# Optimization experiments

Hardware: AMD Instinct MI355X
Metric: run time of the kernel (lower is better)

The kernel has to match this reference:

```python
import jax, jax.numpy as jnp
import numpy as np

D = 64       # embedding_dim
N = 10000    # nodes
E = 160000   # edges (avg degree 16)
R = 16       # removals
C = 512      # connected edges scored per removal


def setup_inputs() -> dict:
    key = jax.random.key(0)
    ks = jax.random.split(key, 18)
    coords = jax.random.normal(ks[0], (N, 2), jnp.float32)
    edge_src = jax.random.randint(ks[1], (E,), 0, N, jnp.int32)
    edge_dst = jax.random.randint(ks[2], (E,), 0, N, jnp.int32)
    removal_idx = jax.random.randint(ks[3], (R,), 0, N, jnp.int32)
    conn_eidx = jax.random.randint(ks[4], (R, C), 0, E, jnp.int32)
    s2 = 1.0 / np.sqrt(2.0)
    sD = 1.0 / np.sqrt(D)
    s2D = 1.0 / np.sqrt(2 * D)
    return {
        "coords": coords,
        "W_emb": jax.random.normal(ks[5], (2, D), jnp.float32) * s2,
        "b_emb": jnp.zeros((D,), jnp.float32),
        "W_self0": jax.random.normal(ks[6], (D, D), jnp.float32) * sD,
        "W_neigh0": jax.random.normal(ks[7], (D, D), jnp.float32) * sD,
        "b_gnn0": jnp.zeros((D,), jnp.float32),
        "W_self1": jax.random.normal(ks[8], (D, D), jnp.float32) * sD,
        "W_neigh1": jax.random.normal(ks[9], (D, D), jnp.float32) * sD,
        "b_gnn1": jnp.zeros((D,), jnp.float32),
        "W_edge": jax.random.normal(ks[10], (2 * D, D), jnp.float32) * s2D,
        "b_edge": jnp.zeros((D,), jnp.float32),
        "W_score": jax.random.normal(ks[11], (2 * D, 1), jnp.float32) * s2D,
        "b_score": jnp.zeros((1,), jnp.float32),
        "edge_src": edge_src,
        "edge_dst": edge_dst,
        "removal_idx": removal_idx,
        "conn_eidx": conn_eidx,
    }


def reference(coords, W_emb, b_emb, W_self0, W_neigh0, b_gnn0,
              W_self1, W_neigh1, b_gnn1, W_edge, b_edge, W_score, b_score,
              edge_src, edge_dst, removal_idx, conn_eidx):
    Nn = coords.shape[0]
    h0 = coords @ W_emb + b_emb  # [N, D] init node embedding

    def gnn_layer(h, emask, Ws, Wn, b):
        # masked mean aggregation of neighbor messages, then linear + relu
        msg = h[edge_src] * emask[:, None]                       # [E, D]
        agg = jax.ops.segment_sum(msg, edge_dst, num_segments=Nn)
        deg = jax.ops.segment_sum(emask, edge_dst, num_segments=Nn)
        agg = agg / jnp.maximum(deg, 1.0)[:, None]
        return jax.nn.relu(h @ Ws + agg @ Wn + b)

    def per_removal(r, conn):
        # tempDestroy: mask out removed node's participation in message passing
        nmask = jnp.ones((Nn,), coords.dtype).at[r].set(0.0)
        emask = nmask[edge_src] * nmask[edge_dst]                # [E]
        h = h0
        h = gnn_layer(h, emask, W_self0, W_neigh0, b_gnn0) + h   # residual
        h = gnn_layer(h, emask, W_self1, W_neigh1, b_gnn1) + h
        s, d = edge_src[conn], edge_dst[conn]                    # connected edges
        ef = jax.nn.relu(jnp.concatenate([h[s], h[d]], -1) @ W_edge + b_edge)  # [C, D]
        r_embed = coords[r] @ W_emb + b_emb                      # [D]
        score_in = jnp.concatenate(
            [jnp.broadcast_to(r_embed, (conn.shape[0], r_embed.shape[0])), ef], -1)
        score = score_in @ W_score + b_score                     # [C, 1]
        return jax.nn.softmax(score, axis=0)[:, 0]               # softmax over edges

    return jax.vmap(per_removal)(removal_idx, conn_eidx)         # [R, C]
```

## Files before the change

### kernel.cpp

```cpp
#include <hip/hip_runtime.h>

#define Df 64
#define NN 10000
#define EE 160000
#define RR 16
#define CC 512
#define CAP1 128
#define CAP2 2048
#define NGEMM 157
#define NAGG 2500
#define NEDG 625
#define NSLF 40
#define ND1B 512
#define ND2B 8192

__device__ float g_h0[NN * Df];
__device__ float g_h1b[NN * Df];
__device__ float g_h2b[NN * Df];
__device__ float g_agg[NN * Df];
__device__ float g_zrow[Df];
__device__ __align__(16) float g_W20[128 * Df];
__device__ __align__(16) float g_W21[128 * Df];
__device__ int g_cntI[NN], g_rowI[NN + 1], g_posI[NN], g_csrI[EE];
__device__ int g_m1mask[NN], g_m2mask[NN];
__device__ int g_mark1[RR][NN], g_mark2[RR][NN];
__device__ int g_n1[RR], g_n2[RR];
__device__ int g_list1[RR][CAP1], g_list2[RR][CAP2];
__device__ float g_d1[RR][CAP1][Df];
__device__ float g_d2[RR][CAP2][Df];
__device__ float g_score[RR * CC];

__global__ void k_init(const float* __restrict__ coords, const float* __restrict__ We,
                       const float* __restrict__ be, const float* __restrict__ Ws0,
                       const float* __restrict__ Wn0, const float* __restrict__ Ws1,
                       const float* __restrict__ Wn1) {
    int i = blockIdx.x * 256 + threadIdx.x;
    if (i < NN * Df) {
        int n = i >> 6, d = i & 63;
        g_h0[i] = coords[2 * n] * We[d] + coords[2 * n + 1] * We[Df + d] + be[d];
    }
    if (i < NN) { g_cntI[i] = 0; g_m1mask[i] = 0; g_m2mask[i] = 0; }
    if (i < Df) g_zrow[i] = 0.f;
    if (i < 8192) {
        int k = i >> 6, d = i & 63;
        g_W20[i] = (k < 64) ? Ws0[k * 64 + d] : Wn0[(k - 64) * 64 + d];
    } else if (i < 16384) {
        int i2 = i - 8192;
        int k = i2 >> 6, d = i2 & 63;
        g_W21[i2] = (k < 64) ? Ws1[k * 64 + d] : Wn1[(k - 64) * 64 + d];
    }
}

__global__ void k_hist(const int* __restrict__ dst) {
    int e = blockIdx.x * 256 + threadIdx.x;
    if (e < EE) atomicAdd(&g_cntI[dst[e]], 1);
}

__global__ __launch_bounds__(1024) void k_scan() {
    int t = threadIdx.x;
    int lane = t & 63, wv = t >> 6;
    const int PER = 10;
    int base = t * PER;
    int vals[PER]; int loc = 0;
#pragma unroll
    for (int k = 0; k < PER; k++) { int v = base + k; vals[k] = (v < NN) ? g_cntI[v] : 0; loc += vals[k]; }
    int sc = loc;
#pragma unroll
    for (int off = 1; off < 64; off <<= 1) { int x = __shfl_up(sc, off, 64); if (lane >= off) sc += x; }
    __shared__ int wsum[16];
    if (lane == 63) wsum[wv] = sc;
    __syncthreads();
    if (t < 16) {
        int x = wsum[t]; int s2 = x;
#pragma unroll
        for (int off = 1; off < 16; off <<= 1) { int y = __shfl_up(s2, off, 16); if (t >= off) s2 += y; }
        wsum[t] = s2 - x;
    }
    __syncthreads();
    int run = wsum[wv] + (sc - loc);
#pragma unroll
    for (int k = 0; k < PER; k++) {
        int v = base + k;
        if (v < NN) { g_rowI[v] = run; g_posI[v] = run; run += vals[k]; }
    }
    if (t == 1023) g_rowI[NN] = run;
}

__global__ void k_fill(const int* __restrict__ src, const int* __restrict__ dst) {
    int e = blockIdx.x * 256 + threadIdx.x;
    if (e < EE) {
        int p = atomicAdd(&g_posI[dst[e]], 1);
        g_csrI[p] = src[e];
    }
}

__device__ __forceinline__ void compact256(const int* __restrict__ maskArr, int bit,
                                           int* mark, int* list, int* nout, int cap) {
    int t = threadIdx.x;
    int lane = t & 63, wv = t >> 6;
    const int PER = 40;
    int base = t * PER;
    int loc = 0;
    for (int k = 0; k < PER; k++) { int v = base + k; if (v < NN) loc += (maskArr[v] >> bit) & 1; }
    int sc = loc;
#pragma unroll
    for (int off = 1; off < 64; off <<= 1) { int x = __shfl_up(sc, off, 64); if (lane >= off) sc += x; }
    __shared__ int wsum[4];
    if (lane == 63) wsum[wv] = sc;
    __syncthreads();
    if (t == 0) { int a = 0; for (int w2 = 0; w2 < 4; w2++) { int x = wsum[w2]; wsum[w2] = a; a += x; } }
    __syncthreads();
    int run = wsum[wv] + (sc - loc);
    for (int k = 0; k < PER; k++) {
        int v = base + k;
        if (v < NN) {
            int f = (maskArr[v] >> bit) & 1;
            if (f && run < cap) { list[run] = v; mark[v] = run + 1; }
            else mark[v] = 0;
            run += f;
        }
    }
    if (t == 255) *nout = (run < cap) ? run : cap;
}

__device__ __forceinline__ void agg_quad(const float* __restrict__ hin, int b, int tid) {
    int lane = tid & 63, w = tid >> 6;
    int n = b * 4 + w;
    int a0 = g_rowI[n], a1 = g_rowI[n + 1];
    float s0 = 0.f, s1 = 0.f, s2 = 0.f, s3 = 0.f;
    int i = a0;
    for (; i + 4 <= a1; i += 4) {
        int c0 = g_csrI[i], c1 = g_csrI[i + 1], c2 = g_csrI[i + 2], c3 = g_csrI[i + 3];
        s0 += hin[c0 * Df + lane];
        s1 += hin[c1 * Df + lane];
        s2 += hin[c2 * Df + lane];
        s3 += hin[c3 * Df + lane];
    }
    for (; i < a1; i++) s0 += hin[g_csrI[i] * Df + lane];
    float s = (s0 + s1) + (s2 + s3);
    g_agg[n * Df + lane] = s / fmaxf((float)(a1 - a0), 1.f);
}

__device__ __forceinline__ void gemm_tile(const float* __restrict__ hin,
                                          float* __restrict__ hout,
                                          const float* __restrict__ W2,
                                          const float* __restrict__ bias, int m0,
                                          int tid) {
    __shared__ float Xs[32][68];
    __shared__ float Wl[32][64];
    int tx = tid & 15, ty = tid >> 4;
    float acc[4][4];
#pragma unroll
    for (int i = 0; i < 4; i++)
#pragma unroll
        for (int j = 0; j < 4; j++) acc[i][j] = 0.f;

    for (int c = 0; c < 4; c++) {
        const float* src = (c < 2) ? hin : g_agg;
        int kb = (c & 1) * 32;
        int kbase = c * 32;
#pragma unroll
        for (int rep = 0; rep < 2; rep++) {
            int slot = tid + rep * 256;
            int m = slot >> 3, q = slot & 7;
            int n = m0 + m;
            float4 v = make_float4(0.f, 0.f, 0.f, 0.f);
            if (n < NN) v = *(const float4*)&src[n * Df + kb + q * 4];
            Xs[q * 4 + 0][m] = v.x; Xs[q * 4 + 1][m] = v.y;
            Xs[q * 4 + 2][m] = v.z; Xs[q * 4 + 3][m] = v.w;
            int k = slot >> 4, dq = slot & 15;
            *(float4*)&Wl[k][dq * 4] = *(const float4*)&W2[(kbase + k) * Df + dq * 4];
        }
        __syncthreads();
#pragma unroll
        for (int k = 0; k < 32; k++) {
            float4 x4 = *(const float4*)&Xs[k][ty * 4];
            float4 w4 = *(const float4*)&Wl[k][tx * 4];
            float xs[4] = {x4.x, x4.y, x4.z, x4.w};
            float ws[4] = {w4.x, w4.y, w4.z, w4.w};
#pragma unroll
            for (int i = 0; i < 4; i++)
#pragma unroll
                for (int j = 0; j < 4; j++) acc[i][j] += xs[i] * ws[j];
        }
        __syncthreads();
    }
    float4 b4 = *(const float4*)&bias[tx * 4];
    float bb[4] = {b4.x, b4.y, b4.z, b4.w};
#pragma unroll
    for (int i = 0; i < 4; i++) {
        int n = m0 + ty * 4 + i;
        if (n < NN) {
            float4 hv = *(const float4*)&hin[n * Df + tx * 4];
            float4 o;
            o.x = fmaxf(acc[i][0] + bb[0], 0.f) + hv.x;
            o.y = fmaxf(acc[i][1] + bb[1], 0.f) + hv.y;
            o.z = fmaxf(acc[i][2] + bb[2], 0.f) + hv.z;
            o.w = fmaxf(acc[i][3] + bb[3], 0.f) + hv.w;
            *(float4*)&hout[n * Df + tx * 4] = o;
        }
    }
}

__global__ __launch_bounds__(256) void k_s1(const int* __restrict__ removal,
                                            const int* __restrict__ esrc,
                                            const int* __restrict__ edst) {
    int b = blockIdx.x, tid = threadIdx.x;
    if (b < NAGG) { agg_quad(g_h0, b, tid); return; }
    if (b < NAGG + NEDG) {
        int e = (b - NAGG) * 256 + tid;
        if (e < EE) {
            int s = esrc[e], d = edst[e];
            int m = 0;
#pragma unroll
            for (int ri = 0; ri < RR; ri++)
                if (s == removal[ri]) m |= (1 << ri);
            if (m) atomicOr(&g_m1mask[d], m);
        }
        return;
    }
    if (tid < RR) atomicOr(&g_m1mask[removal[tid]], 1 << tid);
}

__global__ __launch_bounds__(256) void k_s2(const float* __restrict__ b0,
                                            const int* __restrict__ esrc,
                                            const int* __restrict__ edst) {
    int b = blockIdx.x, tid = threadIdx.x;
    if (b < NGEMM) { gemm_tile(g_h0, g_h1b, g_W20, b0, b * 64, tid); return; }
    if (b < NGEMM + RR) {
        int ri = b - NGEMM;
        compact256(g_m1mask, ri, g_mark1[ri], g_list1[ri], &g_n1[ri], CAP1);
        return;
    }
    if (b < NGEMM + RR + NEDG) {
        int e = (b - NGEMM - RR) * 256 + tid;
        if (e < EE) {
            int m = g_m1mask[esrc[e]];
            if (m) atomicOr(&g_m2mask[edst[e]], m);
        }
        return;
    }
    int v = (b - NGEMM - RR - NEDG) * 256 + tid;
    if (v < NN) {
        int m = g_m1mask[v];
        if (m) atomicOr(&g_m2mask[v], m);
    }
}

__global__ __launch_bounds__(256) void k_s3(const int* __restrict__ removal,
        const float* __restrict__ Ws0, const float* __restrict__ Wn0,
        const float* __restrict__ b0) {
    int b = blockIdx.x, tid = threadIdx.x;
    if (b < NAGG) { agg_quad(g_h1b, b, tid); return; }
    if (b < NAGG + ND1B) {
        __shared__ float s_h[4][Df], s_a[4][Df];
        int rel = b - NAGG;
        int ri = rel >> 5, y = rel & 31;
        int lane = tid & 63, w = tid >> 6;
        int j = y * 4 + w;
        if (j >= g_n1[ri]) return;
        int v = g_list1[ri][j];
        int r = removal[ri];
        float p0s = 0.f, p1s = 0.f, p2s = 0.f, p3s = 0.f; int cnt = 0;
        if (v != r) {
            int e0 = g_rowI[v], e1 = g_rowI[v + 1];
            int i = e0;
            for (; i + 4 <= e1; i += 4) {
                int c0 = g_csrI[i], c1 = g_csrI[i + 1], c2 = g_csrI[i + 2], c3 = g_csrI[i + 3];
                const float* p0 = (c0 == r) ? g_zrow : &g_h0[c0 * Df];
                const float* p1 = (c1 == r) ? g_zrow : &g_h0[c1 * Df];
                const float* p2 = (c2 == r) ? g_zrow : &g_h0[c2 * Df];
                const float* p3 = (c3 == r) ? g_zrow : &g_h0[c3 * Df];
                p0s += p0[lane]; p1s += p1[lane]; p2s += p2[lane]; p3s += p3[lane];
                cnt += (c0 != r) + (c1 != r) + (c2 != r) + (c3 != r);
            }
            for (; i < e1; i++) {
                int c = g_csrI[i];
                const float* p = (c == r) ? g_zrow : &g_h0[c * Df];
                p0s += p[lane]; cnt += (c != r);
            }
        }
        float aggd = (p0s + p1s) + (p2s + p3s);
        float hv = g_h0[v * Df + lane];
        s_h[w][lane] = hv;
        s_a[w][lane] = aggd / fmaxf((float)cnt, 1.f);
        float acc = b0[lane];
#pragma unroll 16
        for (int k = 0; k < Df; k++)
            acc += s_h[w][k] * Ws0[k * Df + lane] + s_a[w][k] * Wn0[k * Df + lane];
        g_d1[ri][j][lane] = fmaxf(acc, 0.f) + hv;
        return;
    }
    int ri = b - NAGG - ND1B;
    compact256(g_m2mask, ri, g_mark2[ri], g_list2[ri], &g_n2[ri], CAP2);
}

__global__ __launch_bounds__(256) void k_s4(const int* __restrict__ removal,
        const float* __restrict__ Ws1, const float* __restrict__ Wn1,
        const float* __restrict__ b1) {
    int b = blockIdx.x, tid = threadIdx.x;
    if (b < NGEMM) { gemm_tile(g_h1b, g_h2b, g_W21, b1, b * 64, tid); return; }
    __shared__ float s_h[4][Df], s_a[4][Df];
    int rel = b - NGEMM;
    int ri = rel >> 9, y = rel & 511;
    int lane = tid & 63, w = tid >> 6;
    int j = y * 4 + w;
    if (j >= g_n2[ri]) return;
    int v = g_list2[ri][j];
    int r = removal[ri];
    const int* mk1 = g_mark1[ri];
    float p0s = 0.f, p1s = 0.f, p2s = 0.f, p3s = 0.f; int cnt = 0;
    if (v != r) {
        int e0 = g_rowI[v], e1 = g_rowI[v + 1];
        int i = e0;
        for (; i + 4 <= e1; i += 4) {
            int c0 = g_csrI[i], c1 = g_csrI[i + 1], c2 = g_csrI[i + 2], c3 = g_csrI[i + 3];
            int m0 = mk1[c0], m1 = mk1[c1], m2 = mk1[c2], m3 = mk1[c3];
            const float* p0 = (c0 == r) ? g_zrow : (m0 > 0 ? &g_d1[ri][m0 - 1][0] : &g_h1b[c0 * Df]);
            const float* p1 = (c1 == r) ? g_zrow : (m1 > 0 ? &g_d1[ri][m1 - 1][0] : &g_h1b[c1 * Df]);
            const float* p2 = (c2 == r) ? g_zrow : (m2 > 0 ? &g_d1[ri][m2 - 1][0] : &g_h1b[c2 * Df]);
            const float* p3 = (c3 == r) ? g_zrow : (m3 > 0 ? &g_d1[ri][m3 - 1][0] : &g_h1b[c3 * Df]);
            p0s += p0[lane]; p1s += p1[lane]; p2s += p2[lane]; p3s += p3[lane];
            cnt += (c0 != r) + (c1 != r) + (c2 != r) + (c3 != r);
        }
        for (; i < e1; i++) {
            int c = g_csrI[i];
            int m = mk1[c];
            const float* p = (c == r) ? g_zrow : (m > 0 ? &g_d1[ri][m - 1][0] : &g_h1b[c * Df]);
            p0s += p[lane]; cnt += (c != r);
        }
    }
    float aggd = (p0s + p1s) + (p2s + p3s);
    int mv = mk1[v];
    float hv = (mv > 0) ? g_d1[ri][mv - 1][lane] : g_h1b[v * Df + lane];
    s_h[w][lane] = hv;
    s_a[w][lane] = aggd / fmaxf((float)cnt, 1.f);
    float acc = b1[lane];
#pragma unroll 16
    for (int k = 0; k < Df; k++)
        acc += s_h[w][k] * Ws1[k * Df + lane] + s_a[w][k] * Wn1[k * Df + lane];
    g_d2[ri][j][lane] = fmaxf(acc, 0.f) + hv;
}

__global__ __launch_bounds__(256) void k_score(const int* __restrict__ conn,
        const int* __restrict__ removal, const int* __restrict__ esrc,
        const int* __restrict__ edst, const float* __restrict__ We,
        const float* __restrict__ be, const float* __restrict__ Wsc,
        const float* __restrict__ bsc) {
    __shared__ const float* ptrs[128];
    __shared__ float Xs[32][68];
    __shared__ float Wl[32][64];
    __shared__ float su;
    int tid = threadIdx.x;
    int e0 = blockIdx.x * 64;
    int ri = e0 >> 9;

    if (tid < 64) {
        int e = conn[e0 + tid];
        int s = esrc[e], d = edst[e];
        int ms = g_mark2[ri][s], md = g_mark2[ri][d];
        ptrs[tid]      = (ms > 0) ? &g_d2[ri][ms - 1][0] : &g_h2b[s * Df];
        ptrs[64 + tid] = (md > 0) ? &g_d2[ri][md - 1][0] : &g_h2b[d * Df];
    } else if (tid < 128) {
        int lane = tid & 63;
        float up = g_h0[removal[ri] * Df + lane] * Wsc[lane];
#pragma unroll
        for (int off = 32; off > 0; off >>= 1) up += __shfl_xor(up, off, 64);
        if (lane == 0) su = up;
    }
    __syncthreads();

    int tx = tid & 15, ty = tid >> 4;
    float acc[4][4];
#pragma unroll
    for (int i = 0; i < 4; i++)
#pragma unroll
        for (int j = 0; j < 4; j++) acc[i][j] = 0.f;

    for (int c = 0; c < 4; c++) {
        int kb = (c & 1) * 32;
#pragma unroll
        for (int rep = 0; rep < 2; rep++) {
            int slot = tid + rep * 256;
            int m = slot >> 3, q = slot & 7;
            const float* p = ((c < 2) ? ptrs[m] : ptrs[64 + m]) + kb + q * 4;
            float4 v = *(const float4*)p;
            Xs[q * 4 + 0][m] = v.x; Xs[q * 4 + 1][m] = v.y;
            Xs[q * 4 + 2][m] = v.z; Xs[q * 4 + 3][m] = v.w;
            int k = slot >> 4, dq = slot & 15;
            *(float4*)&Wl[k][dq * 4] = *(const float4*)&We[(c * 32 + k) * Df + dq * 4];
        }
        __syncthreads();
#pragma unroll
        for (int k = 0; k < 32; k++) {
            float4 x4 = *(const float4*)&Xs[k][ty * 4];
            float4 w4 = *(const float4*)&Wl[k][tx * 4];
            float xs[4] = {x4.x, x4.y, x4.z, x4.w};
            float ws[4] = {w4.x, w4.y, w4.z, w4.w};
#pragma unroll
            for (int i = 0; i < 4; i++)
#pragma unroll
                for (int j = 0; j < 4; j++) acc[i][j] += xs[i] * ws[j];
        }
        __syncthreads();
    }

    float4 be4 = *(const float4*)&be[tx * 4];
    float4 w2  = *(const float4*)&Wsc[Df + tx * 4];
    float bb[4] = {be4.x, be4.y, be4.z, be4.w};
    float ww[4] = {w2.x, w2.y, w2.z, w2.w};
    float sb = su + bsc[0];
#pragma unroll
    for (int i = 0; i < 4; i++) {
        float part = 0.f;
#pragma unroll
        for (int j = 0; j < 4; j++) part += fmaxf(acc[i][j] + bb[j], 0.f) * ww[j];
#pragma unroll
        for (int off = 1; off < 16; off <<= 1) part += __shfl_xor(part, off, 64);
        if (tx == 0) g_score[e0 + ty * 4 + i] = part + sb;
    }
}

__global__ void k_softmax(float* __restrict__ out) {
    int r = blockIdx.x;
    int t = threadIdx.x;
    float v0 = g_score[r * CC + t];
    float v1 = g_score[r * CC + 256 + t];
    __shared__ float red[256];
    red[t] = fmaxf(v0, v1);
    __syncthreads();
    for (int off = 128; off > 0; off >>= 1) {
        if (t < off) red[t] = fmaxf(red[t], red[t + off]);
        __syncthreads();
    }
    float mx = red[0];
    __syncthreads();
    float e0 = expf(v0 - mx), e1 = expf(v1 - mx);
    red[t] = e0 + e1;
    __syncthreads();
    for (int off = 128; off > 0; off >>= 1) {
        if (t < off) red[t] += red[t + off];
        __syncthreads();
    }
    float inv = 1.f / red[0];
    out[r * CC + t] = e0 * inv;
    out[r * CC + 256 + t] = e1 * inv;
}

extern "C" void kernel_launch(void* const* d_in, const int* in_sizes, int n_in,
                              void* d_out, int out_size, void* d_ws, size_t ws_size,
                              hipStream_t stream) {
    const float* coords   = (const float*)d_in[0];
    const float* W_emb    = (const float*)d_in[1];
    const float* b_emb    = (const float*)d_in[2];
    const float* W_self0  = (const float*)d_in[3];
    const float* W_neigh0 = (const float*)d_in[4];
    const float* b_gnn0   = (const float*)d_in[5];
    const float* W_self1  = (const float*)d_in[6];
    const float* W_neigh1 = (const float*)d_in[7];
    const float* b_gnn1   = (const float*)d_in[8];
    const float* W_edge   = (const float*)d_in[9];
    const float* b_edge   = (const float*)d_in[10];
    const float* W_score  = (const float*)d_in[11];
    const float* b_score  = (const float*)d_in[12];
    const int* esrc       = (const int*)d_in[13];
    const int* edst       = (const int*)d_in[14];
    const int* removal    = (const int*)d_in[15];
    const int* conn       = (const int*)d_in[16];

    k_init<<<2500, 256, 0, stream>>>(coords, W_emb, b_emb, W_self0, W_neigh0,
                                     W_self1, W_neigh1);
    k_hist<<<NEDG, 256, 0, stream>>>(edst);
    k_scan<<<1, 1024, 0, stream>>>();
    k_fill<<<NEDG, 256, 0, stream>>>(esrc, edst);

    k_s1<<<NAGG + NEDG + 1, 256, 0, stream>>>(removal, esrc, edst);
    k_s2<<<NGEMM + RR + NEDG + NSLF, 256, 0, stream>>>(b_gnn0, esrc, edst);
    k_s3<<<NAGG + ND1B + RR, 256, 0, stream>>>(removal, W_self0, W_neigh0, b_gnn0);
    k_s4<<<NGEMM + ND2B, 256, 0, stream>>>(removal, W_self1, W_neigh1, b_gnn1);

    k_score<<<RR * CC / 64, 256, 0, stream>>>(conn, removal, esrc, edst,
                                              W_edge, b_edge, W_score, b_score);
    k_softmax<<<RR, 256, 0, stream>>>((float*)d_out);
}
```

Before: 132.8 us.

## Fuse pipeline into one cooperative persistent kernel with grid syncs

```diff
diff --git a/kernel.cpp b/kernel.cpp
--- a/kernel.cpp
+++ b/kernel.cpp
@@ -1,4 +1,7 @@
 #include <hip/hip_runtime.h>
+#include <hip/hip_cooperative_groups.h>
+
+namespace cg = cooperative_groups;
 
 #define Df 64
 #define NN 10000
@@ -13,6 +16,7 @@
 #define NSLF 40
 #define ND1B 512
 #define ND2B 8192
+#define NTHR 256
 
 __device__ float g_h0[NN * Df];
 __device__ float g_h1b[NN * Df];
@@ -30,72 +34,32 @@
 __device__ float g_d2[RR][CAP2][Df];
 __device__ float g_score[RR * CC];
 
-__global__ void k_init(const float* __restrict__ coords, const float* __restrict__ We,
-                       const float* __restrict__ be, const float* __restrict__ Ws0,
-                       const float* __restrict__ Wn0, const float* __restrict__ Ws1,
-                       const float* __restrict__ Wn1) {
-    int i = blockIdx.x * 256 + threadIdx.x;
-    if (i < NN * Df) {
-        int n = i >> 6, d = i & 63;
-        g_h0[i] = coords[2 * n] * We[d] + coords[2 * n + 1] * We[Df + d] + be[d];
-    }
-    if (i < NN) { g_cntI[i] = 0; g_m1mask[i] = 0; g_m2mask[i] = 0; }
-    if (i < Df) g_zrow[i] = 0.f;
-    if (i < 8192) {
-        int k = i >> 6, d = i & 63;
-        g_W20[i] = (k < 64) ? Ws0[k * 64 + d] : Wn0[(k - 64) * 64 + d];
-    } else if (i < 16384) {
-        int i2 = i - 8192;
-        int k = i2 >> 6, d = i2 & 63;
-        g_W21[i2] = (k < 64) ? Ws1[k * 64 + d] : Wn1[(k - 64) * 64 + d];
-    }
-}
-
-__global__ void k_hist(const int* __restrict__ dst) {
-    int e = blockIdx.x * 256 + threadIdx.x;
-    if (e < EE) atomicAdd(&g_cntI[dst[e]], 1);
-}
-
-__global__ __launch_bounds__(1024) void k_scan() {
+__device__ void scan_csr(void) {
     int t = threadIdx.x;
     int lane = t & 63, wv = t >> 6;
-    const int PER = 10;
+    const int PER = 40;
     int base = t * PER;
-    int vals[PER]; int loc = 0;
-#pragma unroll
-    for (int k = 0; k < PER; k++) { int v = base + k; vals[k] = (v < NN) ? g_cntI[v] : 0; loc += vals[k]; }
+    int loc = 0;
+    for (int k = 0; k < PER; k++) { int v = base + k; if (v < NN) loc += g_cntI[v]; }
     int sc = loc;
 #pragma unroll
     for (int off = 1; off < 64; off <<= 1) { int x = __shfl_up(sc, off, 64); if (lane >= off) sc += x; }
-    __shared__ int wsum[16];
-    if (lane == 63) wsum[wv] = sc;
-    __syncthreads();
-    if (t < 16) {
-        int x = wsum[t]; int s2 = x;
-#pragma unroll
-        for (int off = 1; off < 16; off <<= 1) { int y = __shfl_up(s2, off, 16); if (t >= off) s2 += y; }
-        wsum[t] = s2 - x;
-    }
-    __syncthreads();
-    int run = wsum[wv] + (sc - loc);
-#pragma unroll
+    __shared__ int wsumS[4];
+    if (lane == 63) wsumS[wv] = sc;
+    __syncthreads();
+    if (t == 0) { int a = 0; for (int w2 = 0; w2 < 4; w2++) { int x = wsumS[w2]; wsumS[w2] = a; a += x; } }
+    __syncthreads();
+    int run = wsumS[wv] + (sc - loc);
     for (int k = 0; k < PER; k++) {
         int v = base + k;
-        if (v < NN) { g_rowI[v] = run; g_posI[v] = run; run += vals[k]; }
-    }
-    if (t == 1023) g_rowI[NN] = run;
-}
-
-__global__ void k_fill(const int* __restrict__ src, const int* __restrict__ dst) {
-    int e = blockIdx.x * 256 + threadIdx.x;
-    if (e < EE) {
-        int p = atomicAdd(&g_posI[dst[e]], 1);
-        g_csrI[p] = src[e];
-    }
-}
-
-__device__ __forceinline__ void compact256(const int* __restrict__ maskArr, int bit,
-                                           int* mark, int* list, int* nout, int cap) {
+        if (v < NN) { g_rowI[v] = run; g_posI[v] = run; run += g_cntI[v]; }
+    }
+    if (t == 255) g_rowI[NN] = run;
+    __syncthreads();
+}
+
+__device__ void compact256(const int* __restrict__ maskArr, int bit,
+                           int* mark, int* list, int* nout, int cap) {
     int t = threadIdx.x;
     int lane = t & 63, wv = t >> 6;
     const int PER = 40;
@@ -105,12 +69,12 @@
     int sc = loc;
 #pragma unroll
     for (int off = 1; off < 64; off <<= 1) { int x = __shfl_up(sc, off, 64); if (lane >= off) sc += x; }
-    __shared__ int wsum[4];
-    if (lane == 63) wsum[wv] = sc;
-    __syncthreads();
-    if (t == 0) { int a = 0; for (int w2 = 0; w2 < 4; w2++) { int x = wsum[w2]; wsum[w2] = a; a += x; } }
-    __syncthreads();
-    int run = wsum[wv] + (sc - loc);
+    __shared__ int wsumC[4];
+    if (lane == 63) wsumC[wv] = sc;
+    __syncthreads();
+    if (t == 0) { int a = 0; for (int w2 = 0; w2 < 4; w2++) { int x = wsumC[w2]; wsumC[w2] = a; a += x; } }
+    __syncthreads();
+    int run = wsumC[wv] + (sc - loc);
     for (int k = 0; k < PER; k++) {
         int v = base + k;
         if (v < NN) {
@@ -121,9 +85,10 @@
         }
     }
     if (t == 255) *nout = (run < cap) ? run : cap;
-}
-
-__device__ __forceinline__ void agg_quad(const float* __restrict__ hin, int b, int tid) {
+    __syncthreads();
+}
+
+__device__ void agg_quad(const float* __restrict__ hin, int b, int tid) {
     int lane = tid & 63, w = tid >> 6;
     int n = b * 4 + w;
     int a0 = g_rowI[n], a1 = g_rowI[n + 1];
@@ -141,13 +106,11 @@
     g_agg[n * Df + lane] = s / fmaxf((float)(a1 - a0), 1.f);
 }
 
-__device__ __forceinline__ void gemm_tile(const float* __restrict__ hin,
-                                          float* __restrict__ hout,
-                                          const float* __restrict__ W2,
-                                          const float* __restrict__ bias, int m0,
-                                          int tid) {
-    __shared__ float Xs[32][68];
-    __shared__ float Wl[32][64];
+__device__ void gemm_tile(const float* __restrict__ hin, float* __restrict__ hout,
+                          const float* __restrict__ W2, const float* __restrict__ bias,
+                          int m0, int tid, char* smem) {
+    float (*Xs)[68] = (float(*)[68])smem;
+    float (*Wl)[64] = (float(*)[64])(smem + 8704);
     int tx = tid & 15, ty = tid >> 4;
     float acc[4][4];
 #pragma unroll
@@ -202,106 +165,52 @@
     }
 }
 
-__global__ __launch_bounds__(256) void k_s1(const int* __restrict__ removal,
-                                            const int* __restrict__ esrc,
-                                            const int* __restrict__ edst) {
-    int b = blockIdx.x, tid = threadIdx.x;
-    if (b < NAGG) { agg_quad(g_h0, b, tid); return; }
-    if (b < NAGG + NEDG) {
-        int e = (b - NAGG) * 256 + tid;
-        if (e < EE) {
-            int s = esrc[e], d = edst[e];
-            int m = 0;
-#pragma unroll
-            for (int ri = 0; ri < RR; ri++)
-                if (s == removal[ri]) m |= (1 << ri);
-            if (m) atomicOr(&g_m1mask[d], m);
-        }
-        return;
-    }
-    if (tid < RR) atomicOr(&g_m1mask[removal[tid]], 1 << tid);
-}
-
-__global__ __launch_bounds__(256) void k_s2(const float* __restrict__ b0,
-                                            const int* __restrict__ esrc,
-                                            const int* __restrict__ edst) {
-    int b = blockIdx.x, tid = threadIdx.x;
-    if (b < NGEMM) { gemm_tile(g_h0, g_h1b, g_W20, b0, b * 64, tid); return; }
-    if (b < NGEMM + RR) {
-        int ri = b - NGEMM;
-        compact256(g_m1mask, ri, g_mark1[ri], g_list1[ri], &g_n1[ri], CAP1);
-        return;
-    }
-    if (b < NGEMM + RR + NEDG) {
-        int e = (b - NGEMM - RR) * 256 + tid;
-        if (e < EE) {
-            int m = g_m1mask[esrc[e]];
-            if (m) atomicOr(&g_m2mask[edst[e]], m);
-        }
-        return;
-    }
-    int v = (b - NGEMM - RR - NEDG) * 256 + tid;
-    if (v < NN) {
-        int m = g_m1mask[v];
-        if (m) atomicOr(&g_m2mask[v], m);
-    }
-}
-
-__global__ __launch_bounds__(256) void k_s3(const int* __restrict__ removal,
-        const float* __restrict__ Ws0, const float* __restrict__ Wn0,
-        const float* __restrict__ b0) {
-    int b = blockIdx.x, tid = threadIdx.x;
-    if (b < NAGG) { agg_quad(g_h1b, b, tid); return; }
-    if (b < NAGG + ND1B) {
-        __shared__ float s_h[4][Df], s_a[4][Df];
-        int rel = b - NAGG;
-        int ri = rel >> 5, y = rel & 31;
-        int lane = tid & 63, w = tid >> 6;
-        int j = y * 4 + w;
-        if (j >= g_n1[ri]) return;
-        int v = g_list1[ri][j];
-        int r = removal[ri];
-        float p0s = 0.f, p1s = 0.f, p2s = 0.f, p3s = 0.f; int cnt = 0;
-        if (v != r) {
-            int e0 = g_rowI[v], e1 = g_rowI[v + 1];
-            int i = e0;
-            for (; i + 4 <= e1; i += 4) {
-                int c0 = g_csrI[i], c1 = g_csrI[i + 1], c2 = g_csrI[i + 2], c3 = g_csrI[i + 3];
-                const float* p0 = (c0 == r) ? g_zrow : &g_h0[c0 * Df];
-                const float* p1 = (c1 == r) ? g_zrow : &g_h0[c1 * Df];
-                const float* p2 = (c2 == r) ? g_zrow : &g_h0[c2 * Df];
-                const float* p3 = (c3 == r) ? g_zrow : &g_h0[c3 * Df];
-                p0s += p0[lane]; p1s += p1[lane]; p2s += p2[lane]; p3s += p3[lane];
-                cnt += (c0 != r) + (c1 != r) + (c2 != r) + (c3 != r);
-            }
-            for (; i < e1; i++) {
-                int c = g_csrI[i];
-                const float* p = (c == r) ? g_zrow : &g_h0[c * Df];
-                p0s += p[lane]; cnt += (c != r);
-            }
-        }
-        float aggd = (p0s + p1s) + (p2s + p3s);
-        float hv = g_h0[v * Df + lane];
-        s_h[w][lane] = hv;
-        s_a[w][lane] = aggd / fmaxf((float)cnt, 1.f);
-        float acc = b0[lane];
+__device__ void delta1_blk(int rel, int tid, const int* __restrict__ removal,
+                           const float* __restrict__ Ws, const float* __restrict__ Wn,
+                           const float* __restrict__ bias, char* smem) {
+    float* s_h = (float*)smem;
+    float* s_a = s_h + 4 * Df;
+    int ri = rel >> 5, y = rel & 31;
+    int lane = tid & 63, w = tid >> 6;
+    int j = y * 4 + w;
+    if (j >= g_n1[ri]) return;
+    int v = g_list1[ri][j];
+    int r = removal[ri];
+    float p0s = 0.f, p1s = 0.f, p2s = 0.f, p3s = 0.f; int cnt = 0;
+    if (v != r) {
+        int e0 = g_rowI[v], e1 = g_rowI[v + 1];
+        int i = e0;
+        for (; i + 4 <= e1; i += 4) {
+            int c0 = g_csrI[i], c1 = g_csrI[i + 1], c2 = g_csrI[i + 2], c3 = g_csrI[i + 3];
+            const float* p0 = (c0 == r) ? g_zrow : &g_h0[c0 * Df];
+            const float* p1 = (c1 == r) ? g_zrow : &g_h0[c1 * Df];
+            const float* p2 = (c2 == r) ? g_zrow : &g_h0[c2 * Df];
+            const float* p3 = (c3 == r) ? g_zrow : &g_h0[c3 * Df];
+            p0s += p0[lane]; p1s += p1[lane]; p2s += p2[lane]; p3s += p3[lane];
+            cnt += (c0 != r) + (c1 != r) + (c2 != r) + (c3 != r);
+        }
+        for (; i < e1; i++) {
+            int c = g_csrI[i];
+            const float* p = (c == r) ? g_zrow : &g_h0[c * Df];
+            p0s += p[lane]; cnt += (c != r);
+        }
+    }
+    float aggd = (p0s + p1s) + (p2s + p3s);
+    float hv = g_h0[v * Df + lane];
+    s_h[w * Df + lane] = hv;
+    s_a[w * Df + lane] = aggd / fmaxf((float)cnt, 1.f);
+    float acc = bias[lane];
 #pragma unroll 16
-        for (int k = 0; k < Df; k++)
-            acc += s_h[w][k] * Ws0[k * Df + lane] + s_a[w][k] * Wn0[k * Df + lane];
-        g_d1[ri][j][lane] = fmaxf(acc, 0.f) + hv;
-        return;
-    }
-    int ri = b - NAGG - ND1B;
-    compact256(g_m2mask, ri, g_mark2[ri], g_list2[ri], &g_n2[ri], CAP2);
-}
-
-__global__ __launch_bounds__(256) void k_s4(const int* __restrict__ removal,
-        const float* __restrict__ Ws1, const float* __restrict__ Wn1,
-        const float* __restrict__ b1) {
-    int b = blockIdx.x, tid = threadIdx.x;
-    if (b < NGEMM) { gemm_tile(g_h1b, g_h2b, g_W21, b1, b * 64, tid); return; }
-    __shared__ float s_h[4][Df], s_a[4][Df];
-    int rel = b - NGEMM;
+    for (int k = 0; k < Df; k++)
+        acc += s_h[w * Df + k] * Ws[k * Df + lane] + s_a[w * Df + k] * Wn[k * Df + lane];
+    g_d1[ri][j][lane] = fmaxf(acc, 0.f) + hv;
+}
+
+__device__ void delta2_blk(int rel, int tid, const int* __restrict__ removal,
+                           const float* __restrict__ Ws, const float* __restrict__ Wn,
+                           const float* __restrict__ bias, char* smem) {
+    float* s_h = (float*)smem;
+    float* s_a = s_h + 4 * Df;
     int ri = rel >> 9, y = rel & 511;
     int lane = tid & 63, w = tid >> 6;
     int j = y * 4 + w;
@@ -333,26 +242,25 @@
     float aggd = (p0s + p1s) + (p2s + p3s);
     int mv = mk1[v];
     float hv = (mv > 0) ? g_d1[ri][mv - 1][lane] : g_h1b[v * Df + lane];
-    s_h[w][lane] = hv;
-    s_a[w][lane] = aggd / fmaxf((float)cnt, 1.f);
-    float acc = b1[lane];
+    s_h[w * Df + lane] = hv;
+    s_a[w * Df + lane] = aggd / fmaxf((float)cnt, 1.f);
+    float acc = bias[lane];
 #pragma unroll 16
     for (int k = 0; k < Df; k++)
-        acc += s_h[w][k] * Ws1[k * Df + lane] + s_a[w][k] * Wn1[k * Df + lane];
+        acc += s_h[w * Df + k] * Ws[k * Df + lane] + s_a[w * Df + k] * Wn[k * Df + lane];
     g_d2[ri][j][lane] = fmaxf(acc, 0.f) + hv;
 }
 
-__global__ __launch_bounds__(256) void k_score(const int* __restrict__ conn,
-        const int* __restrict__ removal, const int* __restrict__ esrc,
-        const int* __restrict__ edst, const float* __restrict__ We,
-        const float* __restrict__ be, const float* __restrict__ Wsc,
-        const float* __restrict__ bsc) {
-    __shared__ const float* ptrs[128];
-    __shared__ float Xs[32][68];
-    __shared__ float Wl[32][64];
-    __shared__ float su;
-    int tid = threadIdx.x;
-    int e0 = blockIdx.x * 64;
+__device__ void score_blk(int wb, int tid, const int* __restrict__ conn,
+                          const int* __restrict__ removal, const int* __restrict__ esrc,
+                          const int* __restrict__ edst, const float* __restrict__ We,
+                          const float* __restrict__ be, const float* __restrict__ Wsc,
+                          const float* __restrict__ bsc, char* smem) {
+    const float** ptrs = (const float**)smem;
+    float (*Xs)[68] = (float(*)[68])(smem + 1024);
+    float (*Wl)[64] = (float(*)[64])(smem + 1024 + 8704);
+    float* su = (float*)(smem + 1024 + 8704 + 8192);
+    int e0 = wb * 64;
     int ri = e0 >> 9;
 
     if (tid < 64) {
@@ -366,7 +274,7 @@
         float up = g_h0[removal[ri] * Df + lane] * Wsc[lane];
 #pragma unroll
         for (int off = 32; off > 0; off >>= 1) up += __shfl_xor(up, off, 64);
-        if (lane == 0) su = up;
+        if (lane == 0) *su = up;
     }
     __syncthreads();
 
@@ -409,7 +317,7 @@
     float4 w2  = *(const float4*)&Wsc[Df + tx * 4];
     float bb[4] = {be4.x, be4.y, be4.z, be4.w};
     float ww[4] = {w2.x, w2.y, w2.z, w2.w};
-    float sb = su + bsc[0];
+    float sb = *su + bsc[0];
 #pragma unroll
     for (int i = 0; i < 4; i++) {
         float part = 0.f;
@@ -421,30 +329,240 @@
     }
 }
 
-__global__ void k_softmax(float* __restrict__ out) {
-    int r = blockIdx.x;
-    int t = threadIdx.x;
-    float v0 = g_score[r * CC + t];
-    float v1 = g_score[r * CC + 256 + t];
-    __shared__ float red[256];
-    red[t] = fmaxf(v0, v1);
+__device__ void softmax_blk(int r, int tid, float* __restrict__ out, char* smem) {
+    float* red = (float*)smem;
+    float v0 = g_score[r * CC + tid];
+    float v1 = g_score[r * CC + 256 + tid];
+    red[tid] = fmaxf(v0, v1);
     __syncthreads();
     for (int off = 128; off > 0; off >>= 1) {
-        if (t < off) red[t] = fmaxf(red[t], red[t + off]);
+        if (tid < off) red[tid] = fmaxf(red[tid], red[tid + off]);
         __syncthreads();
     }
     float mx = red[0];
     __syncthreads();
     float e0 = expf(v0 - mx), e1 = expf(v1 - mx);
-    red[t] = e0 + e1;
+    red[tid] = e0 + e1;
     __syncthreads();
     for (int off = 128; off > 0; off >>= 1) {
-        if (t < off) red[t] += red[t + off];
+        if (tid < off) red[tid] += red[tid + off];
         __syncthreads();
     }
     float inv = 1.f / red[0];
-    out[r * CC + t] = e0 * inv;
-    out[r * CC + 256 + t] = e1 * inv;
+    out[r * CC + tid] = e0 * inv;
+    out[r * CC + 256 + tid] = e1 * inv;
+}
+
+__global__ __launch_bounds__(256, 4) void k_mega(
+        const float* __restrict__ coords, const float* __restrict__ We,
+        const float* __restrict__ be,
+        const float* __restrict__ Ws0, const float* __restrict__ Wn0,
+        const float* __restrict__ b0,
+        const float* __restrict__ Ws1, const float* __restrict__ Wn1,
+        const float* __restrict__ b1,
+        const float* __restrict__ Wedge, const float* __restrict__ bedge,
+        const float* __restrict__ Wsc, const float* __restrict__ bsc,
+        const int* __restrict__ esrc, const int* __restrict__ edst,
+        const int* __restrict__ removal, const int* __restrict__ conn,
+        float* __restrict__ out) {
+    __shared__ __align__(16) char smem[18048];
+    cg::grid_group grid = cg::this_grid();
+    const int tid = threadIdx.x;
+    const int bid = blockIdx.x;
+    const int nb = gridDim.x;
+    const int gt = bid * NTHR + tid;
+    const int gstride = nb * NTHR;
+
+    for (int i = gt; i < NN * Df; i += gstride) {
+        int n = i >> 6, d = i & 63;
+        g_h0[i] = coords[2 * n] * We[d] + coords[2 * n + 1] * We[Df + d] + be[d];
+    }
+    for (int i = gt; i < NN; i += gstride) { g_cntI[i] = 0; g_m1mask[i] = 0; g_m2mask[i] = 0; }
+    if (gt < Df) g_zrow[gt] = 0.f;
+    for (int i = gt; i < 8192; i += gstride) {
+        int k = i >> 6, d = i & 63;
+        g_W20[i] = (k < 64) ? Ws0[k * 64 + d] : Wn0[(k - 64) * 64 + d];
+        g_W21[i] = (k < 64) ? Ws1[k * 64 + d] : Wn1[(k - 64) * 64 + d];
+    }
+    grid.sync();
+
+    for (int e = gt; e < EE; e += gstride) {
+        atomicAdd(&g_cntI[edst[e]], 1);
+        int s = esrc[e];
+        int m = 0;
+#pragma unroll
+        for (int ri = 0; ri < RR; ri++)
+            if (s == removal[ri]) m |= (1 << ri);
+        if (m) atomicOr(&g_m1mask[edst[e]], m);
+    }
+    if (gt < RR) atomicOr(&g_m1mask[removal[gt]], 1 << gt);
+    grid.sync();
+
+    if (bid == 0) scan_csr();
+    else if (bid <= RR) {
+        int ri = bid - 1;
+        compact256(g_m1mask, ri, g_mark1[ri], g_list1[ri], &g_n1[ri], CAP1);
+    }
+    grid.sync();
+
+    for (int wb = bid; wb < NEDG + NEDG + NSLF; wb += nb) {
+        if (wb < NEDG) {
+            int e = wb * 256 + tid;
+            if (e < EE) {
+                int p = atomicAdd(&g_posI[edst[e]], 1);
+                g_csrI[p] = esrc[e];
+            }
+        } else if (wb < NEDG + NEDG) {
+            int e = (wb - NEDG) * 256 + tid;
+            if (e < EE) {
+                int m = g_m1mask[esrc[e]];
+                if (m) atomicOr(&g_m2mask[edst[e]], m);
+            }
+        } else {
+            int v = (wb - 2 * NEDG) * 256 + tid;
+            if (v < NN) {
+                int m = g_m1mask[v];
+                if (m) atomicOr(&g_m2mask[v], m);
+            }
+        }
+    }
+    grid.sync();
+
+    for (int wb = bid; wb < RR + ND1B + NAGG; wb += nb) {
+        if (wb < RR) compact256(g_m2mask, wb, g_mark2[wb], g_list2[wb], &g_n2[wb], CAP2);
+        else if (wb < RR + ND1B) delta1_blk(wb - RR, tid, removal, Ws0, Wn0, b0, smem);
+        else agg_quad(g_h0, wb - RR - ND1B, tid);
+    }
+    grid.sync();
+
+    for (int wb = bid; wb < NGEMM; wb += nb)
+        gemm_tile(g_h0, g_h1b, g_W20, b0, wb * 64, tid, smem);
+    grid.sync();
+
+    for (int wb = bid; wb < NAGG + ND2B; wb += nb) {
+        if (wb < NAGG) agg_quad(g_h1b, wb, tid);
+        else delta2_blk(wb - NAGG, tid, removal, Ws1, Wn1, b1, smem);
+    }
+    grid.sync();
+
+    for (int wb = bid; wb < NGEMM; wb += nb)
+        gemm_tile(g_h1b, g_h2b, g_W21, b1, wb * 64, tid, smem);
+    grid.sync();
+
+    for (int wb = bid; wb < RR * CC / 64; wb += nb)
+        score_blk(wb, tid, conn, removal, esrc, edst, Wedge, bedge, Wsc, bsc, smem);
+    grid.sync();
+
+    for (int wb = bid; wb < RR; wb += nb)
+        softmax_blk(wb, tid, out, smem);
+}
+
+__global__ void kf_init(const float* __restrict__ coords, const float* __restrict__ We,
+                        const float* __restrict__ be, const float* __restrict__ Ws0,
+                        const float* __restrict__ Wn0, const float* __restrict__ Ws1,
+                        const float* __restrict__ Wn1) {
+    int i = blockIdx.x * 256 + threadIdx.x;
+    if (i < NN * Df) {
+        int n = i >> 6, d = i & 63;
+        g_h0[i] = coords[2 * n] * We[d] + coords[2 * n + 1] * We[Df + d] + be[d];
+    }
+    if (i < NN) { g_cntI[i] = 0; g_m1mask[i] = 0; g_m2mask[i] = 0; }
+    if (i < Df) g_zrow[i] = 0.f;
+    if (i < 8192) {
+        int k = i >> 6, d = i & 63;
+        g_W20[i] = (k < 64) ? Ws0[k * 64 + d] : Wn0[(k - 64) * 64 + d];
+        g_W21[i] = (k < 64) ? Ws1[k * 64 + d] : Wn1[(k - 64) * 64 + d];
+    }
+}
+
+__global__ void kf_edge1(const int* __restrict__ esrc, const int* __restrict__ edst,
+                         const int* __restrict__ removal) {
+    int e = blockIdx.x * 256 + threadIdx.x;
+    if (e < EE) {
+        int d = edst[e];
+        atomicAdd(&g_cntI[d], 1);
+        int s = esrc[e];
+        int m = 0;
+#pragma unroll
+        for (int ri = 0; ri < RR; ri++)
+            if (s == removal[ri]) m |= (1 << ri);
+        if (m) atomicOr(&g_m1mask[d], m);
+    }
+    if (blockIdx.x == 0 && threadIdx.x < RR)
+        atomicOr(&g_m1mask[removal[threadIdx.x]], 1 << threadIdx.x);
+}
+
+__global__ __launch_bounds__(256) void kf_scan16() {
+    int b = blockIdx.x;
+    if (b == 0) scan_csr();
+    else {
+        int ri = b - 1;
+        compact256(g_m1mask, ri, g_mark1[ri], g_list1[ri], &g_n1[ri], CAP1);
+    }
+}
+
+__global__ void kf_fill2(const int* __restrict__ esrc, const int* __restrict__ edst) {
+    int b = blockIdx.x, tid = threadIdx.x;
+    if (b < NEDG) {
+        int e = b * 256 + tid;
+        if (e < EE) {
+            int p = atomicAdd(&g_posI[edst[e]], 1);
+            g_csrI[p] = esrc[e];
+        }
+    } else if (b < 2 * NEDG) {
+        int e = (b - NEDG) * 256 + tid;
+        if (e < EE) {
+            int m = g_m1mask[esrc[e]];
+            if (m) atomicOr(&g_m2mask[edst[e]], m);
+        }
+    } else {
+        int v = (b - 2 * NEDG) * 256 + tid;
+        if (v < NN) {
+            int m = g_m1mask[v];
+            if (m) atomicOr(&g_m2mask[v], m);
+        }
+    }
+}
+
+__global__ __launch_bounds__(256) void kf_p4(const int* __restrict__ removal,
+        const float* __restrict__ Ws0, const float* __restrict__ Wn0,
+        const float* __restrict__ b0) {
+    __shared__ __align__(16) char smem[2048];
+    int b = blockIdx.x, tid = threadIdx.x;
+    if (b < RR) compact256(g_m2mask, b, g_mark2[b], g_list2[b], &g_n2[b], CAP2);
+    else if (b < RR + ND1B) delta1_blk(b - RR, tid, removal, Ws0, Wn0, b0, smem);
+    else agg_quad(g_h0, b - RR - ND1B, tid);
+}
+
+__global__ __launch_bounds__(256) void kf_gemm(int layer, const float* __restrict__ bias) {
+    __shared__ __align__(16) char smem[16896];
+    const float* hin = layer ? g_h1b : g_h0;
+    float* hout      = layer ? g_h2b : g_h1b;
+    const float* W2  = layer ? g_W21 : g_W20;
+    gemm_tile(hin, hout, W2, bias, blockIdx.x * 64, threadIdx.x, smem);
+}
+
+__global__ __launch_bounds__(256) void kf_p6(const int* __restrict__ removal,
+        const float* __restrict__ Ws1, const float* __restrict__ Wn1,
+        const float* __restrict__ b1) {
+    __shared__ __align__(16) char smem[2048];
+    int b = blockIdx.x, tid = threadIdx.x;
+    if (b < NAGG) agg_quad(g_h1b, b, tid);
+    else delta2_blk(b - NAGG, tid, removal, Ws1, Wn1, b1, smem);
+}
+
+__global__ __launch_bounds__(256) void kf_score(const int* __restrict__ conn,
+        const int* __restrict__ removal, const int* __restrict__ esrc,
+        const int* __restrict__ edst, const float* __restrict__ We,
+        const float* __restrict__ be, const float* __restrict__ Wsc,
+        const float* __restrict__ bsc) {
+    __shared__ __align__(16) char smem[18048];
+    score_blk(blockIdx.x, threadIdx.x, conn, removal, esrc, edst, We, be, Wsc, bsc, smem);
+}
+
+__global__ void kf_softmax(float* __restrict__ out) {
+    __shared__ __align__(16) char smem[1024];
+    softmax_blk(blockIdx.x, threadIdx.x, out, smem);
 }
 
 extern "C" void kernel_launch(void* const* d_in, const int* in_sizes, int n_in,
@@ -467,19 +585,44 @@
     const int* edst       = (const int*)d_in[14];
     const int* removal    = (const int*)d_in[15];
     const int* conn       = (const int*)d_in[16];
-
-    k_init<<<2500, 256, 0, stream>>>(coords, W_emb, b_emb, W_self0, W_neigh0,
-                                     W_self1, W_neigh1);
-    k_hist<<<NEDG, 256, 0, stream>>>(edst);
-    k_scan<<<1, 1024, 0, stream>>>();
-    k_fill<<<NEDG, 256, 0, stream>>>(esrc, edst);
-
-    k_s1<<<NAGG + NEDG + 1, 256, 0, stream>>>(removal, esrc, edst);
-    k_s2<<<NGEMM + RR + NEDG + NSLF, 256, 0, stream>>>(b_gnn0, esrc, edst);
-    k_s3<<<NAGG + ND1B + RR, 256, 0, stream>>>(removal, W_self0, W_neigh0, b_gnn0);
-    k_s4<<<NGEMM + ND2B, 256, 0, stream>>>(removal, W_self1, W_neigh1, b_gnn1);
-
-    k_score<<<RR * CC / 64, 256, 0, stream>>>(conn, removal, esrc, edst,
-                                              W_edge, b_edge, W_score, b_score);
-    k_softmax<<<RR, 256, 0, stream>>>((float*)d_out);
-}
+    float* outp           = (float*)d_out;
+
+    hipError_t err = hipErrorUnknown;
+    int dev = 0;
+    (void)hipGetDevice(&dev);
+    hipDeviceProp_t props;
+    int numCU = 0;
+    if (hipGetDeviceProperties(&props, dev) == hipSuccess) numCU = props.multiProcessorCount;
+    int maxb = 0;
+    hipError_t oe = hipOccupancyMaxActiveBlocksPerMultiprocessor(
+        &maxb, reinterpret_cast<const void*>(k_mega), NTHR, 0);
+    int nblk = (oe == hipSuccess && maxb > 0 && numCU > 0) ? maxb * numCU : 0;
+    if (nblk > 1024) nblk = 1024;
+    if (nblk >= 64) {
+        void* args[] = {
+            (void*)&coords, (void*)&W_emb, (void*)&b_emb,
+            (void*)&W_self0, (void*)&W_neigh0, (void*)&b_gnn0,
+            (void*)&W_self1, (void*)&W_neigh1, (void*)&b_gnn1,
+            (void*)&W_edge, (void*)&b_edge, (void*)&W_score, (void*)&b_score,
+            (void*)&esrc, (void*)&edst, (void*)&removal, (void*)&conn,
+            (void*)&outp
+        };
+        err = hipLaunchCooperativeKernel(reinterpret_cast<const void*>(k_mega),
+                                         dim3(nblk), dim3(NTHR), args, 0, stream);
+    }
+    if (err == hipSuccess) return;
+    (void)hipGetLastError();
+
+    kf_init<<<2500, 256, 0, stream>>>(coords, W_emb, b_emb, W_self0, W_neigh0,
+                                      W_self1, W_neigh1);
+    kf_edge1<<<NEDG, 256, 0, stream>>>(esrc, edst, removal);
+    kf_scan16<<<RR + 1, 256, 0, stream>>>();
+    kf_fill2<<<2 * NEDG + NSLF, 256, 0, stream>>>(esrc, edst);
+    kf_p4<<<RR + ND1B + NAGG, 256, 0, stream>>>(removal, W_self0, W_neigh0, b_gnn0);
+    kf_gemm<<<NGEMM, 256, 0, stream>>>(0, b_gnn0);
+    kf_p6<<<NAGG + ND2B, 256, 0, stream>>>(removal, W_self1, W_neigh1, b_gnn1);
+    kf_gemm<<<NGEMM, 256, 0, stream>>>(1, b_gnn1);
+    kf_score<<<RR * CC / 64, 256, 0, stream>>>(conn, removal, esrc, edst,
+                                               W_edge, b_edge, W_score, b_score);
+    kf_softmax<<<RR, 256, 0, stream>>>(outp);
+}
```

New measurement: 515.3 us. 3.88x slower.
